# Kernel tuning notes

Hardware: AMD Instinct MI355X
Metric: run time of the kernel (lower is better)

The kernel has to match this reference:

```python
import jax, jax.numpy as jnp
import numpy as np

H, D_MODEL, D_K, D_V = 16, 1024, 64, 64
B, L = 4, 2048

def _linear_params(key, in_dim, out_dim):
    kw, kb = jax.random.split(key)
    bound = 1.0 / np.sqrt(in_dim)
    W = jax.random.uniform(kw, (out_dim, in_dim), jnp.float32, -bound, bound)
    b = jax.random.uniform(kb, (out_dim,), jnp.float32, -bound, bound)
    return W, b

def setup_inputs() -> dict:
    key = jax.random.key(0)
    ks = jax.random.split(key, 7)
    V = jax.random.normal(ks[0], (B, L, D_MODEL), jnp.float32)
    K = jax.random.normal(ks[1], (B, L, D_MODEL), jnp.float32)
    Q = jax.random.normal(ks[2], (B, L, D_MODEL), jnp.float32)
    Wv, bv = _linear_params(ks[3], D_MODEL, H * D_V)
    Wk, bk = _linear_params(ks[4], D_MODEL, H * D_K)
    Wq, bq = _linear_params(ks[5], D_MODEL, H * D_K)
    Wo, bo = _linear_params(ks[6], H * D_V, D_MODEL)
    return {"V": V, "K": K, "Q": Q, "Wv": Wv, "bv": bv, "Wk": Wk, "bk": bk,
            "Wq": Wq, "bq": bq, "Wo": Wo, "bo": bo}

def reference(V, K, Q, Wv, bv, Wk, bk, Wq, bq, Wo, bo):
    batch, len1, _ = V.shape
    len2 = Q.shape[1]
    # project and split heads: (b, l, h, d)
    v = (V @ Wv.T + bv).reshape(batch, len1, H, D_V)
    k = (K @ Wk.T + bk).reshape(batch, len1, H, D_K)
    q = (Q @ Wq.T + bq).reshape(batch, len2, H, D_K)
    scale = 1.0 / jnp.sqrt(jnp.asarray(D_K, q.dtype))
    # scores: (b, h, len2, len1)
    scores = jnp.einsum('bqhd,bkhd->bhqk', q, k) * scale
    attn = jax.nn.softmax(scores, axis=-1)
    out = jnp.einsum('bhqk,bkhd->bqhd', attn, v).reshape(batch, len2, H * D_V)
    return out @ Wo.T + bo
```

## Files before the change

### kernel.cpp

```cpp
#include <hip/hip_runtime.h>


typedef __bf16 bf16;
typedef __attribute__((ext_vector_type(8))) __bf16 bf16x8;
typedef __attribute__((ext_vector_type(4))) __bf16 bf16x4;
typedef __attribute__((ext_vector_type(4))) float f32x4;
typedef __attribute__((ext_vector_type(16))) float f32x16;

__global__ __launch_bounds__(256) void cvt_all(
    const float* __restrict__ Q, const float* __restrict__ K, const float* __restrict__ V,
    const float* __restrict__ Wq, const float* __restrict__ Wk,
    const float* __restrict__ Wv, const float* __restrict__ Wo,
    bf16* __restrict__ ws)
{
    int bid = blockIdx.x;
    const float* src;
    bf16* dst;
    int lb;
    if (bid < 4096)       { src = Q;  dst = ws;             lb = bid; }
    else if (bid < 8192)  { src = K;  dst = ws + 8388608;   lb = bid - 4096; }
    else if (bid < 12288) { src = V;  dst = ws + 16777216;  lb = bid - 8192; }
    else if (bid < 12800) { src = Wq; dst = ws + 25165824;  lb = bid - 12288; }
    else if (bid < 13312) { src = Wk; dst = ws + 26214400;  lb = bid - 12800; }
    else if (bid < 13824) { src = Wv; dst = ws + 27262976;  lb = bid - 13312; }
    else                  { src = Wo; dst = ws + 28311552;  lb = bid - 13824; }
    size_t i = ((size_t)lb * 256 + threadIdx.x) * 8;
    f32x4 a = *(const f32x4*)(src + i);
    f32x4 b = *(const f32x4*)(src + i + 4);
    bf16x8 o;
    o[0] = (bf16)a[0]; o[1] = (bf16)a[1]; o[2] = (bf16)a[2]; o[3] = (bf16)a[3];
    o[4] = (bf16)b[0]; o[5] = (bf16)b[1]; o[6] = (bf16)b[2]; o[7] = (bf16)b[3];
    *(bf16x8*)(dst + i) = o;
}

__device__ inline void gld_lds16(const void* g, void* l) {
    __builtin_amdgcn_global_load_lds((const __attribute__((address_space(1))) void*)g,
                                     (__attribute__((address_space(3))) void*)l, 16, 0, 0);
}

__global__ __launch_bounds__(256) void proj_fused(
    const bf16* __restrict__ Xq, const bf16* __restrict__ Xk, const bf16* __restrict__ Xv,
    const bf16* __restrict__ Wqb, const bf16* __restrict__ Wkb, const bf16* __restrict__ Wvb,
    const float* __restrict__ bq, const float* __restrict__ bk, const float* __restrict__ bv,
    bf16* __restrict__ qw, bf16* __restrict__ kw, bf16* __restrict__ vtw)
{
    __shared__ bf16 lA[2][8192];
    __shared__ bf16 lB[2][8192];
    const int z = blockIdx.z;
    const bf16*  A    = z == 0 ? Xq  : (z == 1 ? Xk  : Xv);
    const bf16*  W    = z == 0 ? Wqb : (z == 1 ? Wkb : Wvb);
    const float* bias = z == 0 ? bq  : (z == 1 ? bk  : bv);
    bf16*        out  = z == 0 ? qw  : (z == 1 ? kw  : vtw);
    const float scale = z == 0 ? 0.18033688011112042f : 1.0f;

    const int tid  = threadIdx.x;
    const int wave = tid >> 6, lane = tid & 63;
    const int c = lane & 15, g = lane >> 4;

    const int oid = blockIdx.y * 8 + blockIdx.x;
    const int nid = (oid & 7) * 64 + (oid >> 3);
    const int m0 = (nid >> 3) * 128, n0 = (nid & 7) * 128;

    const int wr = wave >> 1, wc = wave & 1;
    const int srow  = lane >> 3;
    const int scol8 = ((lane & 7) ^ srow) * 8;
    const int c7 = c & 7;

    f32x4 acc[4][4] = {};

#define PSTAGE(kt_, bb)                                                         \
    {                                                                           \
        _Pragma("unroll")                                                       \
        for (int i = 0; i < 4; ++i) {                                           \
            int ca = wave * 4 + i;                                              \
            int arow = ca * 8 + srow;                                           \
            gld_lds16(A + (size_t)(m0 + arow) * 1024 + (kt_) * 64 + scol8,      \
                      &lA[bb][ca * 512]);                                       \
            gld_lds16(W + (size_t)(n0 + arow) * 1024 + (kt_) * 64 + scol8,      \
                      &lB[bb][ca * 512]);                                       \
        }                                                                       \
    }

    PSTAGE(0, 0);
    PSTAGE(1, 1);

    for (int kt = 0; kt < 16; ++kt) {
        const int buf = kt & 1;
        if (kt < 15) {
            asm volatile("s_waitcnt vmcnt(8)" ::: "memory");
        } else {
            asm volatile("s_waitcnt vmcnt(0)" ::: "memory");
        }
        __builtin_amdgcn_s_barrier();
        asm volatile("" ::: "memory");

#pragma unroll
        for (int ks = 0; ks < 2; ++ks) {
            bf16x8 af[4], bfr[4];
#pragma unroll
            for (int m = 0; m < 4; ++m) {
                int r = wr * 64 + m * 16 + c;
                af[m] = *(const bf16x8*)&lA[buf][r * 64 + (((ks * 4 + g) ^ c7) * 8)];
            }
#pragma unroll
            for (int n = 0; n < 4; ++n) {
                int r = wc * 64 + n * 16 + c;
                bfr[n] = *(const bf16x8*)&lB[buf][r * 64 + (((ks * 4 + g) ^ c7) * 8)];
            }
#pragma unroll
            for (int m = 0; m < 4; ++m)
#pragma unroll
                for (int n = 0; n < 4; ++n)
                    acc[m][n] = __builtin_amdgcn_mfma_f32_16x16x32_bf16(af[m], bfr[n], acc[m][n], 0, 0, 0);
        }

        asm volatile("" ::: "memory");
        __builtin_amdgcn_s_barrier();
        asm volatile("" ::: "memory");
        if (kt + 2 < 16) PSTAGE(kt + 2, buf);
    }
#undef PSTAGE

#pragma unroll
    for (int m = 0; m < 4; ++m) {
#pragma unroll
        for (int n = 0; n < 4; ++n) {
            int col  = n0 + wc * 64 + n * 16 + c;
            float bb = bias[col];
#pragma unroll
            for (int r = 0; r < 4; ++r) {
                int row = m0 + wr * 64 + m * 16 + 4 * g + r;
                float v = (acc[m][n][r] + bb) * scale;
                int b = row >> 11, l = row & 2047, hh = col >> 6, d = col & 63;
                size_t base = (size_t)(b * 16 + hh) * 131072;
                if (z < 2) {
                    out[base + (l >> 5) * 2048 + (d >> 4) * 512 +
                        ((d >> 3) & 1) * 256 + (l & 31) * 8 + (d & 7)] = (bf16)v;
                } else {
                    out[base + (l >> 5) * 2048 + (d >> 5) * 1024 +
                        ((l >> 4) & 1) * 512 + ((l >> 3) & 1) * 256 +
                        (d & 31) * 8 + (l & 7)] = (bf16)v;
                }
            }
        }
    }
}

__global__ __launch_bounds__(256) void gemm_out(
    const bf16* __restrict__ A, const bf16* __restrict__ W,
    const float* __restrict__ bias, float* __restrict__ out)
{
    __shared__ bf16 lA[2][8192];
    __shared__ bf16 lB[2][8192];
    const int tid  = threadIdx.x;
    const int wave = tid >> 6, lane = tid & 63;
    const int c = lane & 15, g = lane >> 4;

    const int oid = blockIdx.y * 8 + blockIdx.x;
    const int nid = (oid & 7) * 64 + (oid >> 3);
    const int m0 = (nid >> 3) * 128, n0 = (nid & 7) * 128;

    const int wr = wave >> 1, wc = wave & 1;
    const int srow  = lane >> 3;
    const int scol8 = ((lane & 7) ^ srow) * 8;
    const int c7 = c & 7;

    f32x4 acc[4][4] = {};

#define OSTAGE(kt_, bb)                                                         \
    {                                                                           \
        _Pragma("unroll")                                                       \
        for (int i = 0; i < 4; ++i) {                                           \
            int ca = wave * 4 + i;                                              \
            int arow = ca * 8 + srow;                                           \
            gld_lds16(A + (size_t)(m0 + arow) * 1024 + (kt_) * 64 + scol8,      \
                      &lA[bb][ca * 512]);                                       \
            gld_lds16(W + (size_t)(n0 + arow) * 1024 + (kt_) * 64 + scol8,      \
                      &lB[bb][ca * 512]);                                       \
        }                                                                       \
    }

    OSTAGE(0, 0);
    OSTAGE(1, 1);

    for (int kt = 0; kt < 16; ++kt) {
        const int buf = kt & 1;
        if (kt < 15) {
            asm volatile("s_waitcnt vmcnt(8)" ::: "memory");
        } else {
            asm volatile("s_waitcnt vmcnt(0)" ::: "memory");
        }
        __builtin_amdgcn_s_barrier();
        asm volatile("" ::: "memory");

#pragma unroll
        for (int ks = 0; ks < 2; ++ks) {
            bf16x8 af[4], bfr[4];
#pragma unroll
            for (int m = 0; m < 4; ++m) {
                int r = wr * 64 + m * 16 + c;
                af[m] = *(const bf16x8*)&lA[buf][r * 64 + (((ks * 4 + g) ^ c7) * 8)];
            }
#pragma unroll
            for (int n = 0; n < 4; ++n) {
                int r = wc * 64 + n * 16 + c;
                bfr[n] = *(const bf16x8*)&lB[buf][r * 64 + (((ks * 4 + g) ^ c7) * 8)];
            }
#pragma unroll
            for (int m = 0; m < 4; ++m)
#pragma unroll
                for (int n = 0; n < 4; ++n)
                    acc[m][n] = __builtin_amdgcn_mfma_f32_16x16x32_bf16(af[m], bfr[n], acc[m][n], 0, 0, 0);
        }

        asm volatile("" ::: "memory");
        __builtin_amdgcn_s_barrier();
        asm volatile("" ::: "memory");
        if (kt + 2 < 16) OSTAGE(kt + 2, buf);
    }
#undef OSTAGE

#pragma unroll
    for (int m = 0; m < 4; ++m) {
#pragma unroll
        for (int n = 0; n < 4; ++n) {
            int col  = n0 + wc * 64 + n * 16 + c;
            float bb = bias[col];
#pragma unroll
            for (int r = 0; r < 4; ++r) {
                int row = m0 + wr * 64 + m * 16 + 4 * g + r;
                out[(size_t)row * 1024 + col] = acc[m][n][r] + bb;
            }
        }
    }
}

__device__ inline unsigned cvtpk(float lo, float hi) {
    unsigned r;
    asm("v_cvt_pk_bf16_f32 %0, %1, %2" : "=v"(r) : "v"(lo), "v"(hi));
    return r;
}
__device__ inline void pswap(unsigned &a, unsigned &b) {
    asm("v_permlane32_swap_b32 %0, %1" : "+v"(a), "+v"(b));
}

__global__ __launch_bounds__(512) void attn_kernel(
    const bf16* __restrict__ q, const bf16* __restrict__ k,
    const bf16* __restrict__ vt, bf16* __restrict__ O)
{
    __shared__ bf16 lkv[3][4096];
    const int tid  = threadIdx.x;
    const int wave = tid >> 6, lane = tid & 63;
    const int l31 = lane & 31, hi = lane >> 5;
    const int orig = blockIdx.x;
    const int swz  = (orig & 7) * 64 + (orig >> 3);
    const int bh = swz >> 3;
    const int q0 = (swz & 7) * 256 + wave * 32;
    const int laneoff = hi * 256 + l31 * 8;

    const bf16* qb = q  + (size_t)bh * 131072 + (q0 >> 5) * 2048 + laneoff;
    const bf16* kb = k  + (size_t)bh * 131072;
    const bf16* vb = vt + (size_t)bh * 131072;

    bf16x8 qf0 = *(const bf16x8*)(qb);
    bf16x8 qf1 = *(const bf16x8*)(qb + 512);
    bf16x8 qf2 = *(const bf16x8*)(qb + 1024);
    bf16x8 qf3 = *(const bf16x8*)(qb + 1536);

    const bf16* sg = (wave < 4) ? (kb + wave * 512 + lane * 8)
                                : (vb + (wave - 4) * 512 + lane * 8);
    const int   sl = (wave < 4) ? wave * 512 : 2048 + (wave - 4) * 512;

    bf16x8 ones;
#pragma unroll
    for (int i = 0; i < 8; ++i) ones[i] = (bf16)1.0f;

    f32x16 acc0 = {}, acc1 = {}, accS = {};

    gld_lds16(sg,        &lkv[0][sl]);
    gld_lds16(sg + 2048, &lkv[1][sl]);

    int cur = 0;
    for (int t = 0; t < 64; ++t) {
        if (t < 63) {
            asm volatile("s_waitcnt vmcnt(1)" ::: "memory");
        } else {
            asm volatile("s_waitcnt vmcnt(0)" ::: "memory");
        }
        __syncthreads();
        if (t + 2 < 64) {
            int nb = cur + 2; if (nb >= 3) nb -= 3;
            gld_lds16(sg + (size_t)(t + 2) * 2048, &lkv[nb][sl]);
        }

        const bf16* kl = &lkv[cur][laneoff];
        const bf16* vl = &lkv[cur][2048 + laneoff];
        bf16x8 kf0  = *(const bf16x8*)(kl);
        bf16x8 kf1  = *(const bf16x8*)(kl + 512);
        bf16x8 kf2  = *(const bf16x8*)(kl + 1024);
        bf16x8 kf3  = *(const bf16x8*)(kl + 1536);
        bf16x8 vf00 = *(const bf16x8*)(vl);
        bf16x8 vf01 = *(const bf16x8*)(vl + 512);
        bf16x8 vf10 = *(const bf16x8*)(vl + 1024);
        bf16x8 vf11 = *(const bf16x8*)(vl + 1536);

        f32x16 st = {};
        __builtin_amdgcn_s_setprio(1);
        st = __builtin_amdgcn_mfma_f32_32x32x16_bf16(kf0, qf0, st, 0, 0, 0);
        st = __builtin_amdgcn_mfma_f32_32x32x16_bf16(kf1, qf1, st, 0, 0, 0);
        st = __builtin_amdgcn_mfma_f32_32x32x16_bf16(kf2, qf2, st, 0, 0, 0);
        st = __builtin_amdgcn_mfma_f32_32x32x16_bf16(kf3, qf3, st, 0, 0, 0);
        __builtin_amdgcn_s_setprio(0);

#pragma unroll
        for (int r = 0; r < 16; ++r) st[r] = __builtin_amdgcn_exp2f(st[r]);

        unsigned u01 = cvtpk(st[0],  st[1]),  u23 = cvtpk(st[2],  st[3]);
        unsigned u45 = cvtpk(st[4],  st[5]),  u67 = cvtpk(st[6],  st[7]);
        unsigned u89 = cvtpk(st[8],  st[9]),  uAB = cvtpk(st[10], st[11]);
        unsigned uCD = cvtpk(st[12], st[13]), uEF = cvtpk(st[14], st[15]);
        pswap(u01, u45); pswap(u23, u67);
        pswap(u89, uCD); pswap(uAB, uEF);
        union { unsigned u[4]; bf16x8 v; } pf0, pf1;
        pf0.u[0] = u01; pf0.u[1] = u23; pf0.u[2] = u45; pf0.u[3] = u67;
        pf1.u[0] = u89; pf1.u[1] = uAB; pf1.u[2] = uCD; pf1.u[3] = uEF;

        __builtin_amdgcn_s_setprio(1);
        acc0 = __builtin_amdgcn_mfma_f32_32x32x16_bf16(vf00, pf0.v, acc0, 0, 0, 0);
        acc1 = __builtin_amdgcn_mfma_f32_32x32x16_bf16(vf10, pf0.v, acc1, 0, 0, 0);
        accS = __builtin_amdgcn_mfma_f32_32x32x16_bf16(ones, pf0.v, accS, 0, 0, 0);
        acc0 = __builtin_amdgcn_mfma_f32_32x32x16_bf16(vf01, pf1.v, acc0, 0, 0, 0);
        acc1 = __builtin_amdgcn_mfma_f32_32x32x16_bf16(vf11, pf1.v, acc1, 0, 0, 0);
        accS = __builtin_amdgcn_mfma_f32_32x32x16_bf16(ones, pf1.v, accS, 0, 0, 0);
        __builtin_amdgcn_s_setprio(0);

        cur = (cur == 2) ? 0 : cur + 1;
    }

    float inv = 1.0f / accS[0];
    int qg = q0 + l31;
    bf16* ob = O + ((size_t)(bh >> 4) * 2048 + qg) * 1024 + (size_t)(bh & 15) * 64;
#pragma unroll
    for (int rg = 0; rg < 4; ++rg) {
        bf16x4 w0, w1;
#pragma unroll
        for (int i = 0; i < 4; ++i) {
            w0[i] = (bf16)(acc0[rg * 4 + i] * inv);
            w1[i] = (bf16)(acc1[rg * 4 + i] * inv);
        }
        *(bf16x4*)(ob + 8 * rg + 4 * hi)      = w0;
        *(bf16x4*)(ob + 32 + 8 * rg + 4 * hi) = w1;
    }
}

extern "C" void kernel_launch(void* const* d_in, const int* in_sizes, int n_in,
                              void* d_out, int out_size, void* d_ws, size_t ws_size,
                              hipStream_t stream) {
    (void)in_sizes; (void)n_in; (void)out_size; (void)ws_size;
    const float* V  = (const float*)d_in[0];
    const float* K  = (const float*)d_in[1];
    const float* Q  = (const float*)d_in[2];
    const float* Wv = (const float*)d_in[3];
    const float* bv = (const float*)d_in[4];
    const float* Wk = (const float*)d_in[5];
    const float* bk = (const float*)d_in[6];
    const float* Wq = (const float*)d_in[7];
    const float* bq = (const float*)d_in[8];
    const float* Wo = (const float*)d_in[9];
    const float* bo = (const float*)d_in[10];

    char* ws = (char*)d_ws;
    const size_t MB = 1ull << 20;
    bf16* Xq  = (bf16*)(ws + 0);
    bf16* Xk  = (bf16*)(ws + 16 * MB);
    bf16* Xv  = (bf16*)(ws + 32 * MB);
    bf16* Wqb = (bf16*)(ws + 48 * MB);
    bf16* Wkb = (bf16*)(ws + 50 * MB);
    bf16* Wvb = (bf16*)(ws + 52 * MB);
    bf16* Wob = (bf16*)(ws + 54 * MB);
    bf16* qw  = (bf16*)(ws + 56 * MB);
    bf16* kw  = (bf16*)(ws + 72 * MB);
    bf16* vtw = (bf16*)(ws + 88 * MB);
    bf16* Ow  = (bf16*)(ws + 0);

    cvt_all<<<14336, 256, 0, stream>>>(Q, K, V, Wq, Wk, Wv, Wo, (bf16*)ws);

    proj_fused<<<dim3(8, 64, 3), 256, 0, stream>>>(
        Xq, Xk, Xv, Wqb, Wkb, Wvb, bq, bk, bv, qw, kw, vtw);

    attn_kernel<<<512, 512, 0, stream>>>(qw, kw, vtw, Ow);

    gemm_out<<<dim3(8, 64), 256, 0, stream>>>(Ow, Wob, bo, (float*)d_out);
}
```

Before: 185.7 us.

## Enlarge projection GEMM tiles to 256x256 with triple-buffered K=32 pipeline

```diff
diff --git a/kernel.cpp b/kernel.cpp
--- a/kernel.cpp
+++ b/kernel.cpp
@@ -38,15 +38,24 @@
                                      (__attribute__((address_space(3))) void*)l, 16, 0, 0);
 }
 
-__global__ __launch_bounds__(256) void proj_fused(
+__global__ __launch_bounds__(512, 2) void proj_fused(
     const bf16* __restrict__ Xq, const bf16* __restrict__ Xk, const bf16* __restrict__ Xv,
     const bf16* __restrict__ Wqb, const bf16* __restrict__ Wkb, const bf16* __restrict__ Wvb,
     const float* __restrict__ bq, const float* __restrict__ bk, const float* __restrict__ bv,
     bf16* __restrict__ qw, bf16* __restrict__ kw, bf16* __restrict__ vtw)
 {
-    __shared__ bf16 lA[2][8192];
-    __shared__ bf16 lB[2][8192];
-    const int z = blockIdx.z;
+    __shared__ bf16 lA[3][8192];
+    __shared__ bf16 lB[3][8192];
+
+    const int bid = blockIdx.x;
+    const int xcd = bid & 7, idx = bid >> 3;
+    const int chunk = idx >> 3, within = idx & 7;
+    const int gc = xcd * 6 + chunk;
+    const int z  = gc >> 4;
+    const int mp = gc & 15;
+    const int m0 = (mp * 2 + (within >> 2)) * 256;
+    const int n0 = (within & 3) * 256;
+
     const bf16*  A    = z == 0 ? Xq  : (z == 1 ? Xk  : Xv);
     const bf16*  W    = z == 0 ? Wqb : (z == 1 ? Wkb : Wvb);
     const float* bias = z == 0 ? bq  : (z == 1 ? bk  : bv);
@@ -56,80 +65,77 @@
     const int tid  = threadIdx.x;
     const int wave = tid >> 6, lane = tid & 63;
     const int c = lane & 15, g = lane >> 4;
-
-    const int oid = blockIdx.y * 8 + blockIdx.x;
-    const int nid = (oid & 7) * 64 + (oid >> 3);
-    const int m0 = (nid >> 3) * 128, n0 = (nid & 7) * 128;
-
-    const int wr = wave >> 1, wc = wave & 1;
-    const int srow  = lane >> 3;
-    const int scol8 = ((lane & 7) ^ srow) * 8;
-    const int c7 = c & 7;
-
-    f32x4 acc[4][4] = {};
-
-#define PSTAGE(kt_, bb)                                                         \
+    const int wm = wave >> 2, wn = wave & 3;
+
+    const int srow = lane >> 2;
+    const int scol = ((lane & 3) ^ ((lane >> 3) & 3)) * 8;
+    const int rsw  = (g ^ ((c >> 1) & 3)) * 8;
+
+    f32x4 acc[8][4] = {};
+
+#define SA(kt_, bb)                                                             \
     {                                                                           \
         _Pragma("unroll")                                                       \
-        for (int i = 0; i < 4; ++i) {                                           \
-            int ca = wave * 4 + i;                                              \
-            int arow = ca * 8 + srow;                                           \
-            gld_lds16(A + (size_t)(m0 + arow) * 1024 + (kt_) * 64 + scol8,      \
-                      &lA[bb][ca * 512]);                                       \
-            gld_lds16(W + (size_t)(n0 + arow) * 1024 + (kt_) * 64 + scol8,      \
-                      &lB[bb][ca * 512]);                                       \
-        }                                                                       \
-    }
-
-    PSTAGE(0, 0);
-    PSTAGE(1, 1);
-
-    for (int kt = 0; kt < 16; ++kt) {
-        const int buf = kt & 1;
-        if (kt < 15) {
-            asm volatile("s_waitcnt vmcnt(8)" ::: "memory");
+        for (int j = 0; j < 2; ++j)                                             \
+            gld_lds16(A + (size_t)(m0 + j * 128 + wave * 16 + srow) * 1024 +    \
+                          (kt_) * 32 + scol,                                    \
+                      &lA[bb][j * 4096 + wave * 512]);                          \
+    }
+#define SB(kt_, bb)                                                             \
+    {                                                                           \
+        _Pragma("unroll")                                                       \
+        for (int j = 0; j < 2; ++j)                                             \
+            gld_lds16(W + (size_t)(n0 + j * 128 + wave * 16 + srow) * 1024 +    \
+                          (kt_) * 32 + scol,                                    \
+                      &lB[bb][j * 4096 + wave * 512]);                          \
+    }
+
+    SA(0, 0); SB(0, 0);
+    SA(1, 1); SB(1, 1);
+
+    int buf = 0;
+    for (int u = 0; u < 32; ++u) {
+        if (u < 31) {
+            asm volatile("s_waitcnt vmcnt(4)" ::: "memory");
         } else {
             asm volatile("s_waitcnt vmcnt(0)" ::: "memory");
         }
         __builtin_amdgcn_s_barrier();
         asm volatile("" ::: "memory");
 
-#pragma unroll
-        for (int ks = 0; ks < 2; ++ks) {
-            bf16x8 af[4], bfr[4];
-#pragma unroll
-            for (int m = 0; m < 4; ++m) {
-                int r = wr * 64 + m * 16 + c;
-                af[m] = *(const bf16x8*)&lA[buf][r * 64 + (((ks * 4 + g) ^ c7) * 8)];
-            }
-#pragma unroll
-            for (int n = 0; n < 4; ++n) {
-                int r = wc * 64 + n * 16 + c;
-                bfr[n] = *(const bf16x8*)&lB[buf][r * 64 + (((ks * 4 + g) ^ c7) * 8)];
-            }
-#pragma unroll
-            for (int m = 0; m < 4; ++m)
-#pragma unroll
-                for (int n = 0; n < 4; ++n)
-                    acc[m][n] = __builtin_amdgcn_mfma_f32_16x16x32_bf16(af[m], bfr[n], acc[m][n], 0, 0, 0);
-        }
-
-        asm volatile("" ::: "memory");
-        __builtin_amdgcn_s_barrier();
-        asm volatile("" ::: "memory");
-        if (kt + 2 < 16) PSTAGE(kt + 2, buf);
-    }
-#undef PSTAGE
-
-#pragma unroll
-    for (int m = 0; m < 4; ++m) {
+        bf16x8 af[8], bfr[4];
+#pragma unroll
+        for (int m = 0; m < 8; ++m)
+            af[m] = *(const bf16x8*)&lA[buf][(wm * 128 + m * 16 + c) * 32 + rsw];
+#pragma unroll
+        for (int n = 0; n < 4; ++n)
+            bfr[n] = *(const bf16x8*)&lB[buf][(wn * 64 + n * 16 + c) * 32 + rsw];
+
+        if (u + 2 < 32) {
+            int nb = buf + 2; if (nb >= 3) nb -= 3;
+            SA(u + 2, nb); SB(u + 2, nb);
+        }
+
+#pragma unroll
+        for (int m = 0; m < 8; ++m)
+#pragma unroll
+            for (int n = 0; n < 4; ++n)
+                acc[m][n] = __builtin_amdgcn_mfma_f32_16x16x32_bf16(af[m], bfr[n], acc[m][n], 0, 0, 0);
+
+        buf = (buf == 2) ? 0 : buf + 1;
+    }
+#undef SA
+#undef SB
+
+#pragma unroll
+    for (int m = 0; m < 8; ++m) {
 #pragma unroll
         for (int n = 0; n < 4; ++n) {
-            int col  = n0 + wc * 64 + n * 16 + c;
+            int col  = n0 + wn * 64 + n * 16 + c;
             float bb = bias[col];
 #pragma unroll
             for (int r = 0; r < 4; ++r) {
-                int row = m0 + wr * 64 + m * 16 + 4 * g + r;
+                int row = m0 + wm * 128 + m * 16 + 4 * g + r;
                 float v = (acc[m][n][r] + bb) * scale;
                 int b = row >> 11, l = row & 2047, hh = col >> 6, d = col & 63;
                 size_t base = (size_t)(b * 16 + hh) * 131072;
@@ -385,7 +391,7 @@
 
     cvt_all<<<14336, 256, 0, stream>>>(Q, K, V, Wq, Wk, Wv, Wo, (bf16*)ws);
 
-    proj_fused<<<dim3(8, 64, 3), 256, 0, stream>>>(
+    proj_fused<<<384, 512, 0, stream>>>(
         Xq, Xk, Xv, Wqb, Wkb, Wvb, bq, bk, bv, qw, kw, vtw);
 
     attn_kernel<<<512, 512, 0, stream>>>(qw, kw, vtw, Ow);
```

New measurement: 203.4 us. 9.5% more time.
